# Kernel optimization log

Measured on AMD Instinct MI355X. Metric: run time of the kernel, lower is better.

## Reference

```python
import jax, jax.numpy as jnp
import numpy as np

B, FIN, H, W = 16, 256, 32, 32
NH, FH = 8, 64
CIN = FIN + 2  # fin + 2 coordinate-grid pos channels
COUT = NH * FH


def setup_inputs() -> dict:
    key = jax.random.key(0)
    ks = jax.random.split(key, 9)
    s = 1.0 / np.sqrt(CIN)
    so = 1.0 / np.sqrt(COUT)
    return {
        "x": jax.random.normal(ks[0], (B, FIN, H, W), dtype=jnp.float32),
        "wq": jax.random.uniform(ks[1], (COUT, CIN), jnp.float32, -s, s),
        "bq": jax.random.uniform(ks[2], (COUT,), jnp.float32, -s, s),
        "wk": jax.random.uniform(ks[3], (COUT, CIN), jnp.float32, -s, s),
        "bk": jax.random.uniform(ks[4], (COUT,), jnp.float32, -s, s),
        "wv": jax.random.uniform(ks[5], (COUT, CIN), jnp.float32, -s, s),
        "bv": jax.random.uniform(ks[6], (COUT,), jnp.float32, -s, s),
        "wo": jax.random.uniform(ks[7], (FIN, COUT), jnp.float32, -so, so),
        "bo": jax.random.uniform(ks[8], (FIN,), jnp.float32, -so, so),
    }


def reference(x, wq, bq, wk, bk, wv, bv, wo, bo):
    b, c, h, w = x.shape
    n = h * w
    # PosEncoding: concat one linspace(-1,1) coordinate channel per spatial dim
    gy, gx = jnp.meshgrid(jnp.linspace(-1.0, 1.0, h), jnp.linspace(-1.0, 1.0, w), indexing="ij")
    pos = jnp.broadcast_to(jnp.stack([gy, gx])[None], (b, 2, h, w)).astype(x.dtype)
    t = jnp.concatenate([x, pos], axis=1).reshape(b, c + 2, n)  # [B, C+2, N]
    # 1x1 convs are per-token GEMMs
    q = (jnp.einsum("oc,bcn->bon", wq, t) + bq[:, None]).reshape(b, NH, FH, n)
    k = (jnp.einsum("oc,bcn->bon", wk, t) + bk[:, None]).reshape(b, NH, FH, n)
    v = (jnp.einsum("oc,bcn->bon", wv, t) + bv[:, None]).reshape(b, NH, FH, n)
    temp = FH ** 0.5
    attn = jax.nn.softmax(jnp.einsum("bhdn,bhdm->bhnm", q, k) / temp, axis=-1)
    o = jnp.einsum("bhnm,bhdm->bhdn", attn, v).reshape(b, NH * FH, n)
    o = jnp.einsum("oc,bcn->bon", wo, o) + bo[:, None]
    return x + o.reshape(b, c, h, w)
```

## Files before the change

kernel.cpp:

```cpp
#include <hip/hip_runtime.h>


typedef unsigned short u16;
typedef unsigned int   u32;
typedef __attribute__((ext_vector_type(8))) short  short8;
typedef __attribute__((ext_vector_type(4))) float  float4_;

#define MFMA16(a, b, c) __builtin_amdgcn_mfma_f32_16x16x32_bf16(a, b, c, 0, 0, 0)

__device__ __forceinline__ float bf2f(u16 u) {
    union { u32 i; float f; } v; v.i = ((u32)u) << 16; return v.f;
}
__device__ __forceinline__ u16 f2bf(float f) {
    union { float f; u32 i; } v; v.f = f;
    u32 r = v.i + 0x7FFFu + ((v.i >> 16) & 1u);
    return (u16)(r >> 16);
}
__device__ __forceinline__ float exp2_fast(float x) {
    float r;
    asm("v_exp_f32 %0, %1" : "=v"(r) : "v"(x));
    return r;
}
__device__ __forceinline__ u32 cvtpk_bf16(float lo, float hi) {
    u32 r;
    asm("v_cvt_pk_bf16_f32 %0, %1, %2" : "=v"(r) : "v"(lo), "v"(hi));
    return r;
}
__device__ __forceinline__ void pl32swap(u32 &x, u32 &y) {
    asm volatile("v_permlane32_swap_b32 %0, %1" : "+v"(x), "+v"(y));
}
__device__ __forceinline__ void pl16swap(u32 &x, u32 &y) {
    asm volatile("v_permlane16_swap_b32 %0, %1" : "+v"(x), "+v"(y));
}

__global__ __launch_bounds__(256) void prep(
    const float* __restrict__ wq, const float* __restrict__ wk,
    const float* __restrict__ wv, const float* __restrict__ x,
    u16* __restrict__ wb, u16* __restrict__ xT)
{
    __shared__ float Lt[64][65];
    const int bid = blockIdx.x;
    const int tid = threadIdx.x;
    if (bid < 512) {
        int i = bid * 256 + tid;
        int o = i >> 8, c = i & 255;
        size_t si = (size_t)o * 258 + c;
        wb[i]          = f2bf(wq[si]);
        wb[131072 + i] = f2bf(wk[si]);
        wb[262144 + i] = f2bf(wv[si]);
    } else {
        int r = bid - 512;
        int n0 = (r & 15) * 64, c0 = ((r >> 4) & 3) * 64, b = r >> 6;
#pragma unroll
        for (int p = 0; p < 4; ++p) {
            int c = p * 16 + (tid >> 4);
            int nn = (tid & 15) * 4;
            float4 v = *(const float4*)&x[((size_t)(b * 256) + c0 + c) * 1024 + n0 + nn];
            Lt[c][nn + 0] = v.x; Lt[c][nn + 1] = v.y;
            Lt[c][nn + 2] = v.z; Lt[c][nn + 3] = v.w;
        }
        __syncthreads();
#pragma unroll
        for (int p = 0; p < 4; ++p) {
            int n = p * 16 + (tid >> 4);
            int cc = (tid & 15) * 4;
            ushort4 st;
            st.x = f2bf(Lt[cc + 0][n]); st.y = f2bf(Lt[cc + 1][n]);
            st.z = f2bf(Lt[cc + 2][n]); st.w = f2bf(Lt[cc + 3][n]);
            *(ushort4*)&xT[((size_t)(b << 10) + n0 + n) * 256 + c0 + cc] = st;
        }
    }
}

__global__ __launch_bounds__(256) void qkv_mfma(
    const u16* __restrict__ xT, const u16* __restrict__ wb,
    const float* __restrict__ wq, const float* __restrict__ wk,
    const float* __restrict__ wv,
    const float* __restrict__ bq, const float* __restrict__ bk,
    const float* __restrict__ bv,
    u16* __restrict__ qkvbuf)
{
    __shared__ u16 Wl[128 * 64];
    __shared__ u16 Tl[128 * 64];
    const int tid = threadIdx.x;
    const int lane = tid & 63, w = tid >> 6;
    const int quad = lane >> 4, m15 = lane & 15;
    const int n0 = blockIdx.x * 128, mt = blockIdx.y, b = blockIdx.z;
    const int mat = mt >> 2;
    const int m0 = mt * 128;
    const float* worig = (mat == 0) ? wq : ((mat == 1) ? wk : wv);
    const float* bias  = (mat == 0) ? bq : ((mat == 1) ? bk : bv);
    const float oscale = (mat == 1) ? 0.1803368801111204f : 1.0f;
    u16* outbuf = qkvbuf + (size_t)mat * 8388608;

    float4_ acc[2][8];
#pragma unroll
    for (int s = 0; s < 2; ++s)
#pragma unroll
        for (int t = 0; t < 8; ++t) acc[s][t] = (float4_){0, 0, 0, 0};

    const int srow = tid >> 2;
    const int sc8  = (tid & 3) * 8;
    const int rdsw = (m15 & 7) << 3;
    const int sw0  = (srow & 7) << 3;

    const u16* wsrc = wb + (size_t)(m0 + srow) * 256 + sc8;
    const u16* tsrc = xT + ((size_t)(b << 10) + n0 + srow) * 256 + sc8;

    {
        short8 w0 = *(const short8*)(wsrc);
        short8 w1 = *(const short8*)(wsrc + 64 * 256);
        short8 t0 = *(const short8*)(tsrc);
        short8 t1 = *(const short8*)(tsrc + 64 * 256);
        *(short8*)&Wl[srow * 64 + (sc8 ^ sw0)]        = w0;
        *(short8*)&Wl[(srow + 64) * 64 + (sc8 ^ sw0)] = w1;
        *(short8*)&Tl[srow * 64 + (sc8 ^ sw0)]        = t0;
        *(short8*)&Tl[(srow + 64) * 64 + (sc8 ^ sw0)] = t1;
    }
    __syncthreads();

#pragma unroll
    for (int k = 0; k < 8; ++k) {
        const int p = k & 1;
        short8 pw0, pw1, pt0, pt1;
        if (k < 7) {
            const int kc = (k + 1) * 32;
            pw0 = *(const short8*)(wsrc + kc);
            pw1 = *(const short8*)(wsrc + 64 * 256 + kc);
            pt0 = *(const short8*)(tsrc + kc);
            pt1 = *(const short8*)(tsrc + 64 * 256 + kc);
        }

        const int cb = p * 32 + quad * 8;
        short8 af0 = *(const short8*)&Wl[(w * 32 + m15) * 64 + (cb ^ rdsw)];
        short8 af1 = *(const short8*)&Wl[(w * 32 + 16 + m15) * 64 + (cb ^ rdsw)];
        __builtin_amdgcn_s_setprio(1);
#pragma unroll
        for (int t = 0; t < 8; ++t) {
            short8 bf = *(const short8*)&Tl[(t * 16 + m15) * 64 + (cb ^ rdsw)];
            acc[0][t] = MFMA16(af0, bf, acc[0][t]);
            acc[1][t] = MFMA16(af1, bf, acc[1][t]);
        }
        __builtin_amdgcn_s_setprio(0);

        if (k < 7) {
            const int pc = (p ^ 1) * 32 + sc8;
            *(short8*)&Wl[srow * 64 + (pc ^ sw0)]        = pw0;
            *(short8*)&Wl[(srow + 64) * 64 + (pc ^ sw0)] = pw1;
            *(short8*)&Tl[srow * 64 + (pc ^ sw0)]        = pt0;
            *(short8*)&Tl[(srow + 64) * 64 + (pc ^ sw0)] = pt1;
        }
        __syncthreads();
    }

#pragma unroll
    for (int s = 0; s < 2; ++s) {
        float wg[4], wx[4], bi[4];
#pragma unroll
        for (int r = 0; r < 4; ++r) {
            int om = (mt & 3) * 128 + w * 32 + s * 16 + quad * 4 + r;
            wg[r] = worig[(size_t)om * 258 + 256];
            wx[r] = worig[(size_t)om * 258 + 257];
            bi[r] = bias[om];
        }
        const int h = (mt & 3) * 2 + ((w * 32 + s * 16) >> 6);
        const int dbase = ((w * 32 + s * 16) & 63) + quad * 4;
#pragma unroll
        for (int t = 0; t < 8; ++t) {
            int n = n0 + t * 16 + m15;
            float gy = -1.0f + 2.0f * (float)(n >> 5) / 31.0f;
            float gx = -1.0f + 2.0f * (float)(n & 31) / 31.0f;
            float v[4];
#pragma unroll
            for (int r = 0; r < 4; ++r)
                v[r] = (acc[s][t][r] + wg[r] * gy + wx[r] * gx + bi[r]) * oscale;
            if (mat != 2) {
                ushort4 st;
                st.x = f2bf(v[0]); st.y = f2bf(v[1]);
                st.z = f2bf(v[2]); st.w = f2bf(v[3]);
                *(ushort4*)&outbuf[((size_t)(b * 8 + h) * 1024 + n) * 64 + dbase] = st;
            } else {
#pragma unroll
                for (int r = 0; r < 4; ++r)
                    outbuf[((size_t)(b * 8 + h) * 64 + dbase + r) * 1024 + n] = f2bf(v[r]);
            }
        }
    }
}

__global__ __launch_bounds__(512) void attn_mfma(
    u16* __restrict__ qbuf, const u16* __restrict__ kbuf,
    const u16* __restrict__ vbuf)
{
    __shared__ u16 Kl[64 * 64];
    __shared__ u16 Vl[64 * 64];

    const int tid = threadIdx.x;
    const int lane = tid & 63, w = tid >> 6;
    const int quad = lane >> 4, m15 = lane & 15;
    const int bh = blockIdx.x;
    const int q0 = blockIdx.y * 256;
    u16* qb = qbuf + (size_t)bh * 65536;
    const u16* kb = kbuf + (size_t)bh * 65536;
    const u16* vb = vbuf + (size_t)bh * 65536;

    short8 qf[2][2];
#pragma unroll
    for (int s = 0; s < 2; ++s) {
        const u16* qr = qb + (size_t)(q0 + w * 32 + s * 16 + m15) * 64 + quad * 8;
        qf[s][0] = *(const short8*)qr;
        qf[s][1] = *(const short8*)(qr + 32);
    }

    float4_ O[2][4];
    float lp[2] = {0.0f, 0.0f};
#pragma unroll
    for (int s = 0; s < 2; ++s)
#pragma unroll
        for (int t = 0; t < 4; ++t) O[s][t] = (float4_){0, 0, 0, 0};

    const int row = tid >> 3, c8 = (tid & 7) * 8;
    const int stsw = c8 ^ ((row & 7) << 3);
    const int rdsw = (m15 & 7) << 3;

    for (int kt0 = 0; kt0 < 1024; kt0 += 64) {
        __syncthreads();
        *(short8*)&Kl[row * 64 + stsw] =
            *(const short8*)(kb + (size_t)(kt0 + row) * 64 + c8);
        *(short8*)&Vl[row * 64 + stsw] =
            *(const short8*)(vb + (size_t)row * 1024 + kt0 + c8);
        __syncthreads();

        float4_ S[2][4];
#pragma unroll
        for (int s = 0; s < 2; ++s)
#pragma unroll
            for (int t = 0; t < 4; ++t) S[s][t] = (float4_){0, 0, 0, 0};
#pragma unroll
        for (int c = 0; c < 2; ++c) {
            short8 kf[4];
#pragma unroll
            for (int t = 0; t < 4; ++t)
                kf[t] = *(const short8*)&Kl[(t * 16 + m15) * 64 +
                                            ((c * 32 + quad * 8) ^ rdsw)];
            __builtin_amdgcn_s_setprio(1);
#pragma unroll
            for (int s = 0; s < 2; ++s)
#pragma unroll
                for (int t = 0; t < 4; ++t)
                    S[s][t] = MFMA16(kf[t], qf[s][c], S[s][t]);
            __builtin_amdgcn_s_setprio(0);
        }

        u32 W0[2][4], W1[2][4];
#pragma unroll
        for (int s = 0; s < 2; ++s) {
            float lsum = 0.0f;
#pragma unroll
            for (int t = 0; t < 4; ++t) {
                float p0 = exp2_fast(S[s][t][0]);
                float p1 = exp2_fast(S[s][t][1]);
                float p2 = exp2_fast(S[s][t][2]);
                float p3 = exp2_fast(S[s][t][3]);
                W0[s][t] = cvtpk_bf16(p0, p1);
                W1[s][t] = cvtpk_bf16(p2, p3);
                lsum += (p0 + p1) + (p2 + p3);
            }
            lp[s] += lsum;
        }

#pragma unroll
        for (int c = 0; c < 2; ++c) {
            short8 av[4];
#pragma unroll
            for (int dt = 0; dt < 4; ++dt)
                av[dt] = *(const short8*)&Vl[(dt * 16 + m15) * 64 +
                                             ((c * 32 + quad * 8) ^ rdsw)];
#pragma unroll
            for (int s = 0; s < 2; ++s) {
                u32 a = W0[s][2 * c], d = W0[s][2 * c + 1];
                pl32swap(a, d); pl16swap(a, d);
                u32 bb = W1[s][2 * c], e = W1[s][2 * c + 1];
                pl32swap(bb, e); pl16swap(bb, e);
                union { u32 u[4]; short8 v; } bpu;
                bpu.u[0] = a; bpu.u[1] = bb; bpu.u[2] = d; bpu.u[3] = e;
                short8 bp = bpu.v;
                __builtin_amdgcn_s_setprio(1);
#pragma unroll
                for (int dt = 0; dt < 4; ++dt)
                    O[s][dt] = MFMA16(av[dt], bp, O[s][dt]);
                __builtin_amdgcn_s_setprio(0);
            }
        }
    }

#pragma unroll
    for (int s = 0; s < 2; ++s) {
        float v = lp[s];
        v += __shfl_xor(v, 16);
        v += __shfl_xor(v, 32);
        float linv = 1.0f / v;
        int n = q0 + w * 32 + s * 16 + m15;
#pragma unroll
        for (int dt = 0; dt < 4; ++dt) {
            ushort4 st;
            st.x = f2bf(O[s][dt][0] * linv);
            st.y = f2bf(O[s][dt][1] * linv);
            st.z = f2bf(O[s][dt][2] * linv);
            st.w = f2bf(O[s][dt][3] * linv);
            *(ushort4*)&qb[(size_t)n * 64 + dt * 16 + quad * 4] = st;
        }
    }
}

__global__ __launch_bounds__(256) void proj_mfma(
    const u16* __restrict__ ao, const float* __restrict__ wo,
    const float* __restrict__ bo, const float* __restrict__ x,
    float* __restrict__ out)
{
    __shared__ u16 Wl[64 * 64];
    __shared__ u16 Tl[64 * 64];
    const int tid = threadIdx.x;
    const int lane = tid & 63, w = tid >> 6;
    const int quad = lane >> 4, m15 = lane & 15;
    const int n0 = blockIdx.x * 64, f0 = blockIdx.y * 64, b = blockIdx.z;

    float4_ acc[4] = {{0,0,0,0},{0,0,0,0},{0,0,0,0},{0,0,0,0}};
    const int row = tid >> 3, c8 = (tid & 7) * 8;
    const int stsw = c8 ^ ((row & 7) << 3);
    const int rdsw = (m15 & 7) << 3;

    for (int cc0 = 0; cc0 < 512; cc0 += 64) {
        __syncthreads();
        const int h = cc0 >> 6;
#pragma unroll
        for (int rr = 0; rr < 64; rr += 32) {
            const float* wsrc = wo + (size_t)(f0 + row + rr) * 512 + cc0 + c8;
            float4 v0 = *(const float4*)wsrc;
            float4 v1 = *(const float4*)(wsrc + 4);
            uint4 pk;
            pk.x = cvtpk_bf16(v0.x, v0.y);
            pk.y = cvtpk_bf16(v0.z, v0.w);
            pk.z = cvtpk_bf16(v1.x, v1.y);
            pk.w = cvtpk_bf16(v1.z, v1.w);
            *(uint4*)&Wl[(row + rr) * 64 + stsw] = pk;
            *(short8*)&Tl[(row + rr) * 64 + stsw] =
                *(const short8*)(ao + ((size_t)((b << 3) + h) * 1024 + n0 + row + rr) * 64 + c8);
        }
        __syncthreads();
#pragma unroll
        for (int c = 0; c < 2; ++c) {
            short8 af = *(const short8*)&Wl[(w * 16 + m15) * 64 +
                                            ((c * 32 + quad * 8) ^ rdsw)];
#pragma unroll
            for (int t = 0; t < 4; ++t) {
                short8 bf = *(const short8*)&Tl[(t * 16 + m15) * 64 +
                                                ((c * 32 + quad * 8) ^ rdsw)];
                acc[t] = MFMA16(af, bf, acc[t]);
            }
        }
    }

    float bi[4];
#pragma unroll
    for (int r = 0; r < 4; ++r) bi[r] = bo[f0 + w * 16 + quad * 4 + r];
#pragma unroll
    for (int t = 0; t < 4; ++t) {
        int n = n0 + t * 16 + m15;
#pragma unroll
        for (int r = 0; r < 4; ++r) {
            int f = f0 + w * 16 + quad * 4 + r;
            size_t idx = ((size_t)(b * 256) + f) * 1024 + n;
            out[idx] = acc[t][r] + bi[r] + x[idx];
        }
    }
}

extern "C" void kernel_launch(void* const* d_in, const int* in_sizes, int n_in,
                              void* d_out, int out_size, void* d_ws, size_t ws_size,
                              hipStream_t stream) {
    const float* x  = (const float*)d_in[0];
    const float* wq = (const float*)d_in[1];
    const float* bq = (const float*)d_in[2];
    const float* wk = (const float*)d_in[3];
    const float* bk = (const float*)d_in[4];
    const float* wv = (const float*)d_in[5];
    const float* bv = (const float*)d_in[6];
    const float* wo = (const float*)d_in[7];
    const float* bo = (const float*)d_in[8];

    u16* qkvbuf = (u16*)d_ws;
    u16* region = qkvbuf + 3 * 8388608;
    u16* xT = region;
    u16* wb = region + 4194304;

    prep<<<1536, 256, 0, stream>>>(wq, wk, wv, x, wb, xT);

    qkv_mfma<<<dim3(8, 12, 16), 256, 0, stream>>>(
        xT, wb, wq, wk, wv, bq, bk, bv, qkvbuf);

    attn_mfma<<<dim3(128, 4), 512, 0, stream>>>(
        qkvbuf, qkvbuf + 8388608, qkvbuf + 16777216);

    proj_mfma<<<dim3(16, 4, 16), 256, 0, stream>>>(qkvbuf, wo, bo, x, (float*)d_out);
}
```

Before: 166.1 us.

## Double-buffer attention K/V tiles with direct global-to-LDS async loads

Replaces the register-staged K/V tile loads in the attention kernel with global_load_lds DMA-style loads into double-buffered shared memory. The next tile is prefetched while the current one is consumed, and the per-tile barrier count drops from two to one. The swizzle moves to the global source address so the LDS layout stays the same. Correctness depends on the barrier ordering with the async LDS writes and on the source-side swizzle matching the read pattern. Shared memory use doubles.

```diff
diff --git a/kernel.cpp b/kernel.cpp
--- a/kernel.cpp
+++ b/kernel.cpp
@@ -7,6 +7,9 @@
 typedef __attribute__((ext_vector_type(4))) float  float4_;
 
 #define MFMA16(a, b, c) __builtin_amdgcn_mfma_f32_16x16x32_bf16(a, b, c, 0, 0, 0)
+#define GLOAD_LDS16(g, l) \
+    __builtin_amdgcn_global_load_lds((const __attribute__((address_space(1))) void*)(g), \
+                                     (__attribute__((address_space(3))) void*)(l), 16, 0, 0)
 
 __device__ __forceinline__ float bf2f(u16 u) {
     union { u32 i; float f; } v; v.i = ((u32)u) << 16; return v.f;
@@ -192,8 +195,8 @@
     u16* __restrict__ qbuf, const u16* __restrict__ kbuf,
     const u16* __restrict__ vbuf)
 {
-    __shared__ u16 Kl[64 * 64];
-    __shared__ u16 Vl[64 * 64];
+    __shared__ __align__(1024) u16 Ksh[2][4096];
+    __shared__ __align__(1024) u16 Vsh[2][4096];
 
     const int tid = threadIdx.x;
     const int lane = tid & 63, w = tid >> 6;
@@ -204,6 +207,9 @@
     const u16* kb = kbuf + (size_t)bh * 65536;
     const u16* vb = vbuf + (size_t)bh * 65536;
 
+    const int lr = lane >> 3, li = lane & 7;
+    const int swoff = (li * 16) ^ (lr << 4);
+
     short8 qf[2][2];
 #pragma unroll
     for (int s = 0; s < 2; ++s) {
@@ -219,17 +225,26 @@
 #pragma unroll
         for (int t = 0; t < 4; ++t) O[s][t] = (float4_){0, 0, 0, 0};
 
-    const int row = tid >> 3, c8 = (tid & 7) * 8;
-    const int stsw = c8 ^ ((row & 7) << 3);
     const int rdsw = (m15 & 7) << 3;
 
+    {
+        const int grow = w * 8 + lr;
+        GLOAD_LDS16((const char*)kb + (size_t)grow * 128 + swoff, &Ksh[0][w * 512]);
+        GLOAD_LDS16((const char*)vb + (size_t)grow * 2048 + swoff, &Vsh[0][w * 512]);
+    }
+    __syncthreads();
+
+    int cur = 0;
     for (int kt0 = 0; kt0 < 1024; kt0 += 64) {
-        __syncthreads();
-        *(short8*)&Kl[row * 64 + stsw] =
-            *(const short8*)(kb + (size_t)(kt0 + row) * 64 + c8);
-        *(short8*)&Vl[row * 64 + stsw] =
-            *(const short8*)(vb + (size_t)row * 1024 + kt0 + c8);
-        __syncthreads();
+        if (kt0 < 960) {
+            const int grow = w * 8 + lr;
+            GLOAD_LDS16((const char*)kb + (size_t)(kt0 + 64 + grow) * 128 + swoff,
+                        &Ksh[cur ^ 1][w * 512]);
+            GLOAD_LDS16((const char*)vb + (size_t)grow * 2048 + (kt0 + 64) * 2 + swoff,
+                        &Vsh[cur ^ 1][w * 512]);
+        }
+        const u16* Kl = &Ksh[cur][0];
+        const u16* Vl = &Vsh[cur][0];
 
         float4_ S[2][4];
 #pragma unroll
@@ -292,6 +307,9 @@
                 __builtin_amdgcn_s_setprio(0);
             }
         }
+
+        __syncthreads();
+        cur ^= 1;
     }
 
 #pragma unroll
```

Result: no change. 163.6 us (-1.5%).

## Double-buffer output projection K-loop with register prefetch and MFMA priority

Applied to the files above, without the earlier changes.

Restructures the output-projection kernel's reduction loop into 32-wide K steps that split the 64-column LDS tile into two halves used as a ping-pong buffer. The next step's weight and attention-output values are prefetched into registers before the MFMAs, then written to the other half afterward, so only one barrier is needed per step. It also raises wave priority around the MFMA block. This aims to hide global load latency behind compute, but it runs twice as many barrier iterations and uses more registers.

```diff
diff --git a/kernel.cpp b/kernel.cpp
--- a/kernel.cpp
+++ b/kernel.cpp
@@ -326,39 +326,55 @@
     const int n0 = blockIdx.x * 64, f0 = blockIdx.y * 64, b = blockIdx.z;
 
     float4_ acc[4] = {{0,0,0,0},{0,0,0,0},{0,0,0,0},{0,0,0,0}};
-    const int row = tid >> 3, c8 = (tid & 7) * 8;
-    const int stsw = c8 ^ ((row & 7) << 3);
+    const int srow = tid >> 2;
+    const int sc8  = (tid & 3) * 8;
+    const int sw0  = (srow & 7) << 3;
     const int rdsw = (m15 & 7) << 3;
 
-    for (int cc0 = 0; cc0 < 512; cc0 += 64) {
+    const float* wsrc = wo + (size_t)(f0 + srow) * 512 + sc8;
+    const u16* tbase = ao + ((size_t)(b << 3) * 1024 + n0 + srow) * 64 + sc8;
+
+    {
+        float4 v0 = *(const float4*)(wsrc);
+        float4 v1 = *(const float4*)(wsrc + 4);
+        uint4 pk;
+        pk.x = cvtpk_bf16(v0.x, v0.y); pk.y = cvtpk_bf16(v0.z, v0.w);
+        pk.z = cvtpk_bf16(v1.x, v1.y); pk.w = cvtpk_bf16(v1.z, v1.w);
+        *(uint4*)&Wl[srow * 64 + (sc8 ^ sw0)] = pk;
+        *(short8*)&Tl[srow * 64 + (sc8 ^ sw0)] = *(const short8*)(tbase);
+    }
+    __syncthreads();
+
+#pragma unroll
+    for (int k = 0; k < 16; ++k) {
+        const int p = k & 1;
+        float4 pv0, pv1; short8 pt;
+        if (k < 15) {
+            const int kc = (k + 1) * 32;
+            pv0 = *(const float4*)(wsrc + kc);
+            pv1 = *(const float4*)(wsrc + kc + 4);
+            pt  = *(const short8*)(tbase + (size_t)(kc >> 6) * 65536 + (kc & 63));
+        }
+
+        const int cb = p * 32 + quad * 8;
+        short8 af = *(const short8*)&Wl[(w * 16 + m15) * 64 + (cb ^ rdsw)];
+        __builtin_amdgcn_s_setprio(1);
+#pragma unroll
+        for (int t = 0; t < 4; ++t) {
+            short8 bf = *(const short8*)&Tl[(t * 16 + m15) * 64 + (cb ^ rdsw)];
+            acc[t] = MFMA16(af, bf, acc[t]);
+        }
+        __builtin_amdgcn_s_setprio(0);
+
+        if (k < 15) {
+            const int pc = ((p ^ 1) * 32 + sc8) ^ sw0;
+            uint4 pk;
+            pk.x = cvtpk_bf16(pv0.x, pv0.y); pk.y = cvtpk_bf16(pv0.z, pv0.w);
+            pk.z = cvtpk_bf16(pv1.x, pv1.y); pk.w = cvtpk_bf16(pv1.z, pv1.w);
+            *(uint4*)&Wl[srow * 64 + pc] = pk;
+            *(short8*)&Tl[srow * 64 + pc] = pt;
+        }
         __syncthreads();
-        const int h = cc0 >> 6;
-#pragma unroll
-        for (int rr = 0; rr < 64; rr += 32) {
-            const float* wsrc = wo + (size_t)(f0 + row + rr) * 512 + cc0 + c8;
-            float4 v0 = *(const float4*)wsrc;
-            float4 v1 = *(const float4*)(wsrc + 4);
-            uint4 pk;
-            pk.x = cvtpk_bf16(v0.x, v0.y);
-            pk.y = cvtpk_bf16(v0.z, v0.w);
-            pk.z = cvtpk_bf16(v1.x, v1.y);
-            pk.w = cvtpk_bf16(v1.z, v1.w);
-            *(uint4*)&Wl[(row + rr) * 64 + stsw] = pk;
-            *(short8*)&Tl[(row + rr) * 64 + stsw] =
-                *(const short8*)(ao + ((size_t)((b << 3) + h) * 1024 + n0 + row + rr) * 64 + c8);
-        }
-        __syncthreads();
-#pragma unroll
-        for (int c = 0; c < 2; ++c) {
-            short8 af = *(const short8*)&Wl[(w * 16 + m15) * 64 +
-                                            ((c * 32 + quad * 8) ^ rdsw)];
-#pragma unroll
-            for (int t = 0; t < 4; ++t) {
-                short8 bf = *(const short8*)&Tl[(t * 16 + m15) * 64 +
-                                                ((c * 32 + quad * 8) ^ rdsw)];
-                acc[t] = MFMA16(af, bf, acc[t]);
-            }
-        }
     }
 
     float bi[4];
```

Measured after the change: 166.6 us. Within noise of the previous version (+0.3%).
